# Optimization experiments

Hardware: AMD Instinct MI355X
Metric: run time of the kernel (lower is better)

## Reference

```python
import jax, jax.numpy as jnp
from jax import lax
import numpy as np

B, IMG_H, IMG_W = 8, 256, 512
NUM_CLASSES, P = 20, 32
SCALE, TOPK, IOU_THR = 32.0, 100, 0.5


def conv2d(x, w, b, stride=1, pad=1):
    y = lax.conv_general_dilated(x, w, (stride, stride), [(pad, pad), (pad, pad)],
                                 dimension_numbers=('NCHW', 'OIHW', 'NCHW'))
    return y + b[None, :, None, None]


def bilinear_resize(img, out_h, out_w):
    # img: [..., H, W]; torch F.interpolate(mode='bilinear', align_corners=False)
    H, W = img.shape[-2], img.shape[-1]
    def idx_w(n_in, n_out):
        src = (jnp.arange(n_out, dtype=jnp.float32) + 0.5) * (n_in / n_out) - 0.5
        src = jnp.clip(src, 0.0, n_in - 1)
        i0 = jnp.floor(src).astype(jnp.int32)
        i1 = jnp.minimum(i0 + 1, n_in - 1)
        return i0, i1, src - i0.astype(jnp.float32)
    y0, y1, wy = idx_w(H, out_h)
    x0, x1, wx = idx_w(W, out_w)
    top = img[..., y0, :] * (1.0 - wy)[:, None] + img[..., y1, :] * wy[:, None]
    return top[..., x0] * (1.0 - wx) + top[..., x1] * wx


def generate_anchors(fh, fw):
    ys = (jnp.arange(fh, dtype=jnp.float32) + 0.5) * (IMG_H / fh)
    xs = (jnp.arange(fw, dtype=jnp.float32) + 0.5) * (IMG_W / fw)
    cy, cx = jnp.meshgrid(ys, xs, indexing='ij')
    h = SCALE / 2
    return jnp.stack([cx - h, cy - h, cx + h, cy + h], -1).reshape(-1, 4)


def delta_to_boxes(anchors, deltas):
    a_c = (anchors[:, :2] + anchors[:, 2:]) / 2
    a_wh = anchors[:, 2:] - anchors[:, :2]
    pc = a_c + deltas[..., :2] * a_wh
    pwh = a_wh * jnp.exp(deltas[..., 2:])
    return jnp.concatenate([pc - pwh / 2, pc + pwh / 2], -1)


def nms_single(boxes, scores, labels):
    # torchvision batched_nms: offset boxes per label, greedy NMS, return kept idxs
    N = boxes.shape[0]
    off = labels.astype(boxes.dtype) * (jnp.max(boxes) + 1.0)
    b = boxes + off[:, None]
    order = jnp.argsort(-scores)
    bs = b[order]
    area = (bs[:, 2] - bs[:, 0]) * (bs[:, 3] - bs[:, 1])
    lt = jnp.maximum(bs[:, None, :2], bs[None, :, :2])
    rb = jnp.minimum(bs[:, None, 2:], bs[None, :, 2:])
    wh = jnp.clip(rb - lt, 0.0)
    inter = wh[..., 0] * wh[..., 1]
    iou = inter / (area[:, None] + area[None, :] - inter + 1e-9)
    idxs = jnp.arange(N)
    def body(i, suppressed):
        keep_i = jnp.logical_not(suppressed[i])
        row = (iou[i] > IOU_THR) & (idxs > i)
        return jnp.where(keep_i, suppressed | row, suppressed)
    suppressed = lax.fori_loop(0, N, body, jnp.zeros(N, bool))
    keep_mask = ~suppressed
    rank = jnp.cumsum(keep_mask) - 1
    slots = jnp.where(keep_mask & (rank < TOPK), rank, TOPK)
    out = jnp.full(TOPK + 1, -1, jnp.int32).at[slots].set(order.astype(jnp.int32))
    return out[:TOPK]


def setup_inputs():
    key = jax.random.key(0)
    ks = jax.random.split(key, 17)
    def cw(k, o, i, kh, kw_):
        return jax.random.normal(k, (o, i, kh, kw_), jnp.float32) / np.sqrt(i * kh * kw_)
    return {
        'images': jax.random.normal(ks[0], (B, 3, IMG_H, IMG_W), jnp.float32),
        'w1': cw(ks[1], 64, 3, 3, 3),   'b1': jnp.zeros(64, jnp.float32),
        'w2': cw(ks[2], 128, 64, 3, 3), 'b2': jnp.zeros(128, jnp.float32),
        'w3': cw(ks[3], 256, 128, 3, 3),'b3': jnp.zeros(256, jnp.float32),
        'pw1': cw(ks[4], 256, 256, 3, 3), 'pb1': jnp.zeros(256, jnp.float32),
        'pw2': cw(ks[5], P, 256, 1, 1),   'pb2': jnp.zeros(P, jnp.float32),
        'cw_': cw(ks[6], NUM_CLASSES + 1, 256, 3, 3), 'cb': jnp.zeros(NUM_CLASSES + 1, jnp.float32),
        'bw': cw(ks[7], 4, 256, 3, 3),  'bb': jnp.zeros(4, jnp.float32),
        'kw': cw(ks[8], P, 256, 3, 3),  'kb': jnp.zeros(P, jnp.float32),
    }


def reference(images, w1, b1, w2, b2, w3, b3, pw1, pb1, pw2, pb2, cw_, cb, bw, bb, kw, kb):
    x = jax.nn.relu(conv2d(images, w1, b1, stride=2))
    x = jax.nn.relu(conv2d(x, w2, b2, stride=2))
    feat = jax.nn.relu(conv2d(x, w3, b3, stride=2))          # [B,256,32,64]
    proto = conv2d(jax.nn.relu(conv2d(feat, pw1, pb1)), pw2, pb2, pad=0)  # [B,P,32,64]
    fh, fw = feat.shape[2], feat.shape[3]
    def head(w, b, c):
        return conv2d(feat, w, b).transpose(0, 2, 3, 1).reshape(B, -1, c)
    cls = head(cw_, cb, NUM_CLASSES + 1)     # [B,N,C+1]
    box = head(bw, bb, 4)                    # [B,N,4]
    coef = head(kw, kb, P)                   # [B,N,P]
    anchors = generate_anchors(fh, fw)       # [N,4]
    probs = jax.nn.softmax(cls, -1)[..., :-1]
    scores = probs.max(-1)
    labels = probs.argmax(-1).astype(jnp.int32)
    boxes = delta_to_boxes(anchors, box)     # [B,N,4]
    keep = jax.vmap(nms_single)(boxes, scores, labels)   # [B,100], -1 pad
    valid = keep >= 0
    ki = jnp.clip(keep, 0)
    take = lambda a: jnp.take_along_axis(a, ki[..., None] if a.ndim == 3 else ki, axis=1)
    boxes_k = take(boxes) * valid[..., None]
    scores_k = take(scores) * valid
    labels_k = jnp.where(valid, take(labels), 0)
    coef_k = jnp.take_along_axis(coef, ki[..., None], axis=1)   # [B,100,P]
    m = jax.nn.sigmoid(jnp.einsum('bkp,bphw->bkhw', coef_k, proto))
    masks = bilinear_resize(m, IMG_H, IMG_W) > 0.5
    masks = masks & valid[..., None, None]
    return boxes_k, scores_k, labels_k, masks, valid
```

## Files before the change

### kernel.cpp

```cpp
#include <hip/hip_runtime.h>
#include <hip/hip_bf16.h>
#include <math.h>

#define BB 8
#define NCLS 21
#define NANCH 2048
#define TOPK_N 100

static const size_t OFF_X1HI = 0;
static const size_t OFF_X1LO = 34344960;
static const size_t OFF_X2HI = 68689920;
static const size_t OFF_X2LO = 86261760;
static const size_t OFF_FTHI = 103833600;
static const size_t OFF_FTLO = 113025024;
static const size_t ZERO_BYTES = 122216448;
static const size_t OFF_WT1  = 122216448;
static const size_t OFF_A2H  = 122223616;
static const size_t OFF_A2L  = 122371072;
static const size_t OFF_A3H  = 122518528;
static const size_t OFF_A3L  = 123108352;
static const size_t OFF_AHH  = 123698176;
static const size_t OFF_AHL  = 123993088;
static const size_t OFF_AP1H = 124288000;
static const size_t OFF_AP1L = 125467648;
static const size_t OFF_WTP2 = 126647296;
static const size_t OFF_BH   = 126680064;
static const size_t OFF_HOUT = 126680576;
static const size_t OFF_P1   = 130874880;
static const size_t OFF_PROTO= 147652096;
static const size_t OFF_BOXES= 149749248;
static const size_t OFF_SCORES=150011392;
static const size_t OFF_LABELS=150076928;
static const size_t OFF_ORDER= 150142464;
static const size_t OFF_SB   = 150208000;
static const size_t OFF_IOU  = 150470144;
static const size_t OFF_KEEP = 154664448;
static const size_t OFF_MAXB = 154668032;
static const size_t OFF_M    = 154668544;

static const size_t OUT_BOXES  = 0;
static const size_t OUT_SCORES = 3200;
static const size_t OUT_LABELS = 4000;
static const size_t OUT_MASKS  = 4800;
static const size_t OUT_VALID  = 104862400;

typedef __attribute__((ext_vector_type(8))) short bf16x8;
typedef __attribute__((ext_vector_type(4))) float f32x4;

__device__ __forceinline__ unsigned encf(float f){
  unsigned u = __float_as_uint(f);
  return (u & 0x80000000u) ? ~u : (u | 0x80000000u);
}
__device__ __forceinline__ float decf(unsigned u){
  unsigned b = (u & 0x80000000u) ? (u & 0x7fffffffu) : ~u;
  return __uint_as_float(b);
}
__device__ __forceinline__ short f2bf(float f){
  __hip_bfloat16 h = __float2bfloat16(f);
  return *(short*)&h;
}
__device__ __forceinline__ float bf2f(short h){
  return __uint_as_float(((unsigned)(unsigned short)h) << 16);
}

__global__ void initk(unsigned* maxb){
  if (threadIdx.x < BB) maxb[threadIdx.x] = 0u;
}

__global__ void zerok(float4* __restrict__ p, long n4){
  long i = (long)blockIdx.x*256 + threadIdx.x;
  if (i < n4) p[i] = make_float4(0.f,0.f,0.f,0.f);
}

template<int CIN,int COUT,int KK>
__global__ void packw(const float* __restrict__ w, float* __restrict__ wT){
  int i = blockIdx.x*256 + threadIdx.x;
  if (i >= CIN*KK*COUT) return;
  int co = i % COUT; int r = i / COUT;
  int ci = r / KK,  k = r % KK;
  wT[i] = w[(co*CIN + ci)*KK + k];
}

template<int CIN,int COUT>
__global__ void packA(const float* __restrict__ w, short* __restrict__ Ahi,
                      short* __restrict__ Alo){
  constexpr int K = CIN*9;
  constexpr int KS = K/32;
  int i = blockIdx.x*256 + threadIdx.x;
  if (i >= COUT*K) return;
  int sub  = i & 7;
  int lane = (i >> 3) & 63;
  int rest = i >> 9;
  int ks = rest % KS;
  int mt = rest / KS;
  int m = mt*16 + (lane & 15);
  int k = ks*32 + (lane >> 4)*8 + sub;
  int tap = k / CIN, ci = k - tap*CIN;
  float v = w[(m*CIN + ci)*9 + tap];
  short h = f2bf(v);
  Ahi[i] = h;
  Alo[i] = f2bf(v - bf2f(h));
}

__global__ void packAh(const float* __restrict__ cw, const float* __restrict__ bw,
                       const float* __restrict__ kw, const float* __restrict__ cb,
                       const float* __restrict__ bb, const float* __restrict__ kb,
                       short* __restrict__ Ahi, short* __restrict__ Alo,
                       float* __restrict__ bh){
  int i = blockIdx.x*256 + threadIdx.x;
  if (i < 64){
    float v = 0.f;
    if (i < 21) v = cb[i]; else if (i < 25) v = bb[i-21]; else if (i < 57) v = kb[i-25];
    bh[i] = v;
  }
  if (i >= 64*2304) return;
  constexpr int KS = 72;
  int sub  = i & 7;
  int lane = (i >> 3) & 63;
  int rest = i >> 9;
  int ks = rest % KS;
  int mt = rest / KS;
  int m = mt*16 + (lane & 15);
  int k = ks*32 + (lane >> 4)*8 + sub;
  int tap = k >> 8, ci = k & 255;
  float v = 0.f;
  if (m < 21)      v = cw[(m*256 + ci)*9 + tap];
  else if (m < 25) v = bw[((m-21)*256 + ci)*9 + tap];
  else if (m < 57) v = kw[((m-25)*256 + ci)*9 + tap];
  short h = f2bf(v);
  Ahi[i] = h;
  Alo[i] = f2bf(v - bf2f(h));
}

__global__ __launch_bounds__(256) void conv1k(const float* __restrict__ img,
    const float* __restrict__ wT, const float* __restrict__ bias,
    short* __restrict__ x1hi, short* __restrict__ x1lo){
  const int b   = blockIdx.z;
  const int co0 = blockIdx.y * 16;
  const int g   = blockIdx.x*256 + threadIdx.x;
  const int y  = g >> 7;
  const int x0 = (g & 127) << 1;

  float acc[16][2];
#pragma unroll
  for (int c=0;c<16;c++){
    float bv = bias[co0+c];
    acc[c][0] = bv; acc[c][1] = bv;
  }
  int   off[3][5];
  float msk[3][5];
#pragma unroll
  for (int kh=0;kh<3;kh++){
    int iy = y*2 - 1 + kh;
    bool okr = (iy >= 0) && (iy < 256);
    int ro = okr ? iy*512 : 0;
#pragma unroll
    for (int t=0;t<5;t++){
      int col = x0*2 - 1 + t;
      bool ok = okr && (col >= 0) && (col < 512);
      off[kh][t] = ok ? (ro + col) : 0;
      msk[kh][t] = ok ? 1.f : 0.f;
    }
  }
  const float* inb = img + (size_t)b*3*256*512;
  for (int ci=0; ci<3; ci++){
    const float* inc = inb + (size_t)ci*256*512;
    float v[3][5];
#pragma unroll
    for (int kh=0;kh<3;kh++)
#pragma unroll
      for (int t=0;t<5;t++)
        v[kh][t] = inc[off[kh][t]] * msk[kh][t];
    const float* wp = wT + ci*9*64 + co0;
#pragma unroll
    for (int kh=0;kh<3;kh++)
#pragma unroll
    for (int kw=0;kw<3;kw++){
      const float* wq = wp + (kh*3+kw)*64;
#pragma unroll
      for (int c=0;c<16;c++){
        float wv = wq[c];
        acc[c][0] = fmaf(wv, v[kh][2*0+kw], acc[c][0]);
        acc[c][1] = fmaf(wv, v[kh][2*1+kw], acc[c][1]);
      }
    }
  }
#pragma unroll
  for (int s=0;s<2;s++){
    short hv[16] __attribute__((aligned(16)));
    short lv[16] __attribute__((aligned(16)));
#pragma unroll
    for (int c=0;c<16;c++){
      float r = fmaxf(acc[c][s], 0.f);
      short h = f2bf(r);
      hv[c] = h;
      lv[c] = f2bf(r - bf2f(h));
    }
#pragma unroll
    for (int g2=0; g2<2; g2++){
      size_t ad = (((size_t)(b*8 + (co0>>3) + g2)*130 + (y+1))*258 + (x0+s+1))*8;
      *(bf16x8*)(x1hi + ad) = *(bf16x8*)(hv + g2*8);
      *(bf16x8*)(x1lo + ad) = *(bf16x8*)(lv + g2*8);
    }
  }
}

template<int CIN,int K,int M,int MW,int NW,int OW,int OHh,int S,int IPH,int IPW,
         bool SPLIT,int EMODE,int OPH,int OPW>
__global__ __launch_bounds__(NW*64) void cgemm(
    const short* __restrict__ Ahi, const short* __restrict__ Alo,
    const short* __restrict__ Bhi, const short* __restrict__ Blo,
    const float* __restrict__ bias, float* __restrict__ outf,
    short* __restrict__ outhi, short* __restrict__ outlo){
  static_assert(CIN % 32 == 0, "CIN must be multiple of 32");
  constexpr int NT = OW*OHh;
  constexpr int KS = K/32;
  constexpr int CG = CIN/8;
  const int b    = blockIdx.z;
  const int wave = threadIdx.x >> 6;
  const int lane = threadIdx.x & 63;
  const int lm = lane & 15, lq = lane >> 4;
  const int m0 = (blockIdx.y * NW + wave) * (MW*16);
  const int n0 = blockIdx.x * 64;

  int oy[4], ox[4];
#pragma unroll
  for (int j=0;j<4;j++){
    int n = n0 + j*16 + lm;
    oy[j] = n / OW; ox[j] = n % OW;
  }

  f32x4 acc[MW][4];
#pragma unroll
  for (int i=0;i<MW;i++)
#pragma unroll
    for (int j=0;j<4;j++) acc[i][j] = (f32x4){0.f,0.f,0.f,0.f};

  const short* Ah_l = Ahi + (size_t)lane*8;
  const short* Al_l = Alo + (size_t)lane*8;
  const int mt0 = m0 >> 4;

  const size_t plane = (size_t)IPH*IPW;
  const short* Bh0 = Bhi + ((size_t)b*CG + lq)*plane*8;
  const short* Bl0 = Blo + ((size_t)b*CG + lq)*plane*8;

#pragma unroll 3
  for (int tap=0; tap<9; tap++){
    const int dy = tap/3, dx = tap%3;
    size_t pix[4];
#pragma unroll
    for (int j=0;j<4;j++)
      pix[j] = (size_t)(oy[j]*S + dy)*IPW + (size_t)(ox[j]*S + dx);
    const int ksb = tap*(CIN/32);
#pragma unroll
    for (int kc=0; kc<CIN; kc+=32){
      const int ks = ksb + (kc>>5);
      const size_t koff = (size_t)(kc>>3)*plane;
      bf16x8 ah[MW], bh_[4];
#pragma unroll
      for (int i=0;i<MW;i++)
        ah[i] = *(const bf16x8*)(Ah_l + ((size_t)(mt0+i)*KS + ks)*512);
#pragma unroll
      for (int j=0;j<4;j++) bh_[j] = *(const bf16x8*)(Bh0 + (koff + pix[j])*8);
      if constexpr (SPLIT){
        bf16x8 al[MW], bl_[4];
#pragma unroll
        for (int i=0;i<MW;i++)
          al[i] = *(const bf16x8*)(Al_l + ((size_t)(mt0+i)*KS + ks)*512);
#pragma unroll
        for (int j=0;j<4;j++) bl_[j] = *(const bf16x8*)(Bl0 + (koff + pix[j])*8);
#pragma unroll
        for (int j=0;j<4;j++)
#pragma unroll
          for (int i=0;i<MW;i++)
            acc[i][j] = __builtin_amdgcn_mfma_f32_16x16x32_bf16(ah[i], bh_[j], acc[i][j], 0,0,0);
#pragma unroll
        for (int j=0;j<4;j++)
#pragma unroll
          for (int i=0;i<MW;i++)
            acc[i][j] = __builtin_amdgcn_mfma_f32_16x16x32_bf16(ah[i], bl_[j], acc[i][j], 0,0,0);
#pragma unroll
        for (int j=0;j<4;j++)
#pragma unroll
          for (int i=0;i<MW;i++)
            acc[i][j] = __builtin_amdgcn_mfma_f32_16x16x32_bf16(al[i], bh_[j], acc[i][j], 0,0,0);
      } else {
#pragma unroll
        for (int j=0;j<4;j++)
#pragma unroll
          for (int i=0;i<MW;i++)
            acc[i][j] = __builtin_amdgcn_mfma_f32_16x16x32_bf16(ah[i], bh_[j], acc[i][j], 0,0,0);
      }
    }
  }

#pragma unroll
  for (int i=0;i<MW;i++){
#pragma unroll
    for (int r=0;r<4;r++){
      const int m = m0 + i*16 + lq*4 + r;
      const float bv = bias[m];
      if constexpr (EMODE == 0){
#pragma unroll
        for (int j=0;j<4;j++){
          float v = fmaxf(acc[i][j][r] + bv, 0.f);
          short h = f2bf(v);
          short l = f2bf(v - bf2f(h));
          size_t ad = ((((size_t)(b*(M/8) + (m>>3))*OPH + (oy[j]+1))*OPW + (ox[j]+1)))*8 + (m&7);
          outhi[ad] = h;
          outlo[ad] = l;
        }
      } else {
        float* cp = outf + ((size_t)b*M + m)*NT + n0 + lm;
#pragma unroll
        for (int j=0;j<4;j++){
          float v = acc[i][j][r] + bv;
          if constexpr (EMODE == 2) v = fmaxf(v, 0.f);
          cp[j*16] = v;
        }
      }
    }
  }
}

__global__ __launch_bounds__(256) void pw2k2(const float* __restrict__ p1,
    const float* __restrict__ wT, const float* __restrict__ bias,
    float* __restrict__ proto){
  const int b  = blockIdx.y;
  const int sp = blockIdx.x*256 + threadIdx.x;
  float acc[32];
#pragma unroll
  for (int c=0;c<32;c++) acc[c] = bias[c];
  const float* pb = p1 + (size_t)b*256*NANCH + sp;
  for (int ci=0;ci<256;ci++){
    float v = pb[(size_t)ci*NANCH];
    const float* wq = wT + ci*32;
#pragma unroll
    for (int c=0;c<32;c++) acc[c] = fmaf(v, wq[c], acc[c]);
  }
#pragma unroll
  for (int c=0;c<32;c++)
    proto[((size_t)b*32 + c)*NANCH + sp] = acc[c];
}

__global__ void decodek(const float* __restrict__ hout,
                        float* __restrict__ boxes, float* __restrict__ scores,
                        int* __restrict__ labels, unsigned* __restrict__ maxb){
  const int b = blockIdx.y;
  const int n = blockIdx.x*blockDim.x + threadIdx.x;
  const float* cp = hout + (size_t)b*64*NANCH + n;
  float l[NCLS];
  float M = -1e30f;
#pragma unroll
  for (int c=0;c<NCLS;c++){ l[c] = cp[(size_t)c*NANCH]; M = fmaxf(M, l[c]); }
  float denom = 0.f;
#pragma unroll
  for (int c=0;c<NCLS;c++) denom += expf(l[c]-M);
  float best = -1.f; int bi = 0;
#pragma unroll
  for (int c=0;c<NCLS-1;c++){
    float e = expf(l[c]-M);
    if (e > best){ best = e; bi = c; }
  }
  scores[(size_t)b*NANCH + n] = best/denom;
  labels[(size_t)b*NANCH + n] = bi;

  float dx = cp[21*(size_t)NANCH], dy = cp[22*(size_t)NANCH];
  float dw = cp[23*(size_t)NANCH], dh = cp[24*(size_t)NANCH];
  const int yy = n >> 6, xx = n & 63;
  float cx = (xx+0.5f)*8.f, cy = (yy+0.5f)*8.f;
  float px = cx + dx*32.f, py = cy + dy*32.f;
  float pw = 32.f*expf(dw), ph = 32.f*expf(dh);
  float x1 = px - 0.5f*pw, y1 = py - 0.5f*ph;
  float x2 = px + 0.5f*pw, y2 = py + 0.5f*ph;
  float* bo = boxes + ((size_t)b*NANCH + n)*4;
  bo[0]=x1; bo[1]=y1; bo[2]=x2; bo[3]=y2;
  float mx = fmaxf(fmaxf(x1,y1), fmaxf(x2,y2));
#pragma unroll
  for (int off=32; off>0; off>>=1) mx = fmaxf(mx, __shfl_down(mx, off));
  if ((threadIdx.x & 63) == 0) atomicMax(maxb + b, encf(mx));
}

__global__ void __launch_bounds__(1024) sortk(const float* __restrict__ scores,
                     const float* __restrict__ boxes, const int* __restrict__ labels,
                     const unsigned* __restrict__ maxb,
                     int* __restrict__ order, float* __restrict__ sb){
  __shared__ float sc[NANCH];
  __shared__ int   id[NANCH];
  const int b = blockIdx.x, t = threadIdx.x;
  for (int i=t;i<NANCH;i+=1024){ sc[i]=scores[(size_t)b*NANCH+i]; id[i]=i; }
  __syncthreads();
  for (int k=2;k<=NANCH;k<<=1){
    for (int j=k>>1;j>0;j>>=1){
      for (int i=t;i<NANCH;i+=1024){
        int ixj = i ^ j;
        if (ixj > i){
          float sa=sc[i], sb_=sc[ixj]; int ia=id[i], ib=id[ixj];
          bool dir = ((i & k) == 0);
          bool before_ba = (sb_ > sa) || (sb_ == sa && ib < ia);
          if (before_ba == dir){ sc[i]=sb_; sc[ixj]=sa; id[i]=ib; id[ixj]=ia; }
        }
      }
      __syncthreads();
    }
  }
  float mboff = decf(maxb[b]) + 1.0f;
  for (int r=t;r<NANCH;r+=1024){
    int o = id[r];
    order[(size_t)b*NANCH + r] = o;
    float off = (float)labels[(size_t)b*NANCH + o] * mboff;
    const float* bo = boxes + ((size_t)b*NANCH + o)*4;
    float* sp = sb + ((size_t)b*NANCH + r)*4;
    sp[0]=bo[0]+off; sp[1]=bo[1]+off; sp[2]=bo[2]+off; sp[3]=bo[3]+off;
  }
}

__global__ void ioumask(const float* __restrict__ sb, unsigned long long* __restrict__ iou){
  const int b = blockIdx.y;
  const int gid = blockIdx.x*blockDim.x + threadIdx.x;
  const int i = gid >> 5, w = gid & 31;
  const float* base = sb + (size_t)b*NANCH*4;
  unsigned long long bits = 0ull;
  const int j0 = w << 6;
  if (j0 + 63 > i){
    float x1=base[i*4], y1=base[i*4+1], x2=base[i*4+2], y2=base[i*4+3];
    float ai = (x2-x1)*(y2-y1);
    for (int jj=0;jj<64;jj++){
      int j = j0 + jj;
      if (j > i){
        float bx1=base[j*4], by1=base[j*4+1], bx2=base[j*4+2], by2=base[j*4+3];
        float lx=fmaxf(x1,bx1), ly=fmaxf(y1,by1);
        float rx=fminf(x2,bx2), ry=fminf(y2,by2);
        float ww=fmaxf(rx-lx,0.f), hh=fmaxf(ry-ly,0.f);
        float inter = ww*hh;
        float aj = (bx2-bx1)*(by2-by1);
        float v = inter/(ai + aj - inter + 1e-9f);
        if (v > 0.5f) bits |= (1ull << jj);
      }
    }
  }
  iou[((size_t)b*NANCH + i)*32 + w] = bits;
}

__global__ void nmsscan(const unsigned long long* __restrict__ iou,
                        const int* __restrict__ order, int* __restrict__ keep){
  const int b = blockIdx.x, lane = threadIdx.x;
  unsigned long long sup = 0ull;
  int k = 0;
  for (int i=0; i<NANCH && k<TOPK_N; i++){
    int wi = i >> 6, bi = i & 63;
    unsigned long long wv = __shfl(sup, wi);
    if (!((wv >> bi) & 1ull)){
      if (lane == 0) keep[b*TOPK_N + k] = order[(size_t)b*NANCH + i];
      k++;
      unsigned long long row = (lane < 32) ? iou[((size_t)b*NANCH + i)*32 + lane] : 0ull;
      sup |= row;
    }
  }
  for (int r = lane; r < TOPK_N; r += 64)
    if (r >= k) keep[b*TOPK_N + r] = -1;
}

__global__ void gatherk(const int* __restrict__ keep, const float* __restrict__ boxes,
                        const float* __restrict__ scores, const int* __restrict__ labels,
                        float* __restrict__ out){
  const int b = blockIdx.x, r = threadIdx.x;
  if (r >= TOPK_N) return;
  int ki = keep[b*TOPK_N + r];
  float valid = (ki >= 0) ? 1.f : 0.f;
  int kc = (ki < 0) ? 0 : ki;
  const float* bo = boxes + ((size_t)b*NANCH + kc)*4;
#pragma unroll
  for (int c=0;c<4;c++) out[OUT_BOXES + ((size_t)b*TOPK_N + r)*4 + c] = bo[c]*valid;
  out[OUT_SCORES + b*TOPK_N + r] = scores[(size_t)b*NANCH + kc]*valid;
  out[OUT_LABELS + b*TOPK_N + r] = (ki >= 0) ? (float)labels[(size_t)b*NANCH + kc] : 0.f;
  out[OUT_VALID  + b*TOPK_N + r] = valid;
}

__global__ void maskm(const int* __restrict__ keep, const float* __restrict__ hout,
                      const float* __restrict__ proto, float* __restrict__ m){
  const int b = blockIdx.z, r = blockIdx.y;
  const int s = blockIdx.x*blockDim.x + threadIdx.x;
  __shared__ float cf[32];
  int ki = keep[b*TOPK_N + r];
  int kc = (ki < 0) ? 0 : ki;
  if (threadIdx.x < 32)
    cf[threadIdx.x] = hout[((size_t)b*64 + 25 + threadIdx.x)*NANCH + kc];
  __syncthreads();
  float acc = 0.f;
#pragma unroll
  for (int p=0;p<32;p++) acc = fmaf(cf[p], proto[((size_t)b*32 + p)*NANCH + s], acc);
  m[((size_t)b*TOPK_N + r)*NANCH + s] = 1.f/(1.f + expf(-acc));
}

__global__ void resizek(const float* __restrict__ m, const int* __restrict__ keep,
                        float* __restrict__ out){
  const int b = blockIdx.z, r = blockIdx.y;
  const int pid = blockIdx.x*blockDim.x + threadIdx.x;
  const int y  = pid >> 7;
  const int x4 = (pid & 127) << 2;
  bool valid = keep[b*TOPK_N + r] >= 0;
  const float* mb = m + ((size_t)b*TOPK_N + r)*NANCH;
  float sy = (y + 0.5f)*0.125f - 0.5f;
  sy = fminf(fmaxf(sy, 0.f), 31.f);
  int y0 = (int)floorf(sy);
  int y1 = min(y0+1, 31);
  float wy = sy - (float)y0;
  const float* r0 = mb + y0*64;
  const float* r1 = mb + y1*64;
  float res[4];
#pragma unroll
  for (int k=0;k<4;k++){
    int x = x4 + k;
    float sx = (x + 0.5f)*0.125f - 0.5f;
    sx = fminf(fmaxf(sx, 0.f), 63.f);
    int x0 = (int)floorf(sx);
    int x1 = min(x0+1, 63);
    float wx = sx - (float)x0;
    float t0 = r0[x0]*(1.f-wy) + r1[x0]*wy;
    float t1 = r0[x1]*(1.f-wy) + r1[x1]*wy;
    float v  = t0*(1.f-wx) + t1*wx;
    res[k] = (v > 0.5f && valid) ? 1.f : 0.f;
  }
  float4 v4 = make_float4(res[0], res[1], res[2], res[3]);
  *(float4*)(out + OUT_MASKS + (((size_t)b*TOPK_N + r)*256 + y)*512 + x4) = v4;
}

extern "C" void kernel_launch(void* const* d_in, const int* in_sizes, int n_in,
                              void* d_out, int out_size, void* d_ws, size_t ws_size,
                              hipStream_t stream) {
  const float* images=(const float*)d_in[0];
  const float* w1=(const float*)d_in[1];  const float* b1=(const float*)d_in[2];
  const float* w2=(const float*)d_in[3];  const float* b2=(const float*)d_in[4];
  const float* w3=(const float*)d_in[5];  const float* b3=(const float*)d_in[6];
  const float* pw1=(const float*)d_in[7]; const float* pb1=(const float*)d_in[8];
  const float* pw2=(const float*)d_in[9]; const float* pb2=(const float*)d_in[10];
  const float* cw=(const float*)d_in[11]; const float* cb=(const float*)d_in[12];
  const float* bw=(const float*)d_in[13]; const float* bb=(const float*)d_in[14];
  const float* kw=(const float*)d_in[15]; const float* kb=(const float*)d_in[16];
  float* out = (float*)d_out;
  char* ws = (char*)d_ws;

  short* x1hi = (short*)(ws + OFF_X1HI);
  short* x1lo = (short*)(ws + OFF_X1LO);
  short* x2hi = (short*)(ws + OFF_X2HI);
  short* x2lo = (short*)(ws + OFF_X2LO);
  short* fthi = (short*)(ws + OFF_FTHI);
  short* ftlo = (short*)(ws + OFF_FTLO);
  float* wT1  = (float*)(ws + OFF_WT1);
  short* a2h  = (short*)(ws + OFF_A2H);
  short* a2l  = (short*)(ws + OFF_A2L);
  short* a3h  = (short*)(ws + OFF_A3H);
  short* a3l  = (short*)(ws + OFF_A3L);
  short* ahh  = (short*)(ws + OFF_AHH);
  short* ahl  = (short*)(ws + OFF_AHL);
  short* ap1h = (short*)(ws + OFF_AP1H);
  short* ap1l = (short*)(ws + OFF_AP1L);
  float* wTp2 = (float*)(ws + OFF_WTP2);
  float* bh   = (float*)(ws + OFF_BH);
  float* hout = (float*)(ws + OFF_HOUT);
  float* p1   = (float*)(ws + OFF_P1);
  float* proto= (float*)(ws + OFF_PROTO);
  float* boxes= (float*)(ws + OFF_BOXES);
  float* scores=(float*)(ws + OFF_SCORES);
  int*   labels=(int*)  (ws + OFF_LABELS);
  int*   order =(int*)  (ws + OFF_ORDER);
  float* sb   = (float*)(ws + OFF_SB);
  unsigned long long* iou = (unsigned long long*)(ws + OFF_IOU);
  int*   keep = (int*)  (ws + OFF_KEEP);
  unsigned* maxb = (unsigned*)(ws + OFF_MAXB);
  float* m    = (float*)(ws + OFF_M);

  initk<<<dim3(1), dim3(64), 0, stream>>>(maxb);

  zerok<<<dim3((unsigned)(ZERO_BYTES/16/256)), 256, 0, stream>>>((float4*)ws, (long)(ZERO_BYTES/16));

  packw<3,64,9>  <<<dim3(7),    256, 0, stream>>>(w1, wT1);
  packA<64,128>  <<<dim3(288),  256, 0, stream>>>(w2, a2h, a2l);
  packA<128,256> <<<dim3(1152), 256, 0, stream>>>(w3, a3h, a3l);
  packA<256,256> <<<dim3(2304), 256, 0, stream>>>(pw1, ap1h, ap1l);
  packAh<<<dim3(576), 256, 0, stream>>>(cw, bw, kw, cb, bb, kb, ahh, ahl, bh);
  packw<256,32,1><<<dim3(32),   256, 0, stream>>>(pw2, wTp2);

  conv1k<<<dim3(64,4,BB), 256, 0, stream>>>(images, wT1, b1, x1hi, x1lo);

  cgemm<64,576,128,4,2,128,64,2,130,258,true,0,66,130>
      <<<dim3(128,1,BB), 128, 0, stream>>>(a2h, a2l, x1hi, x1lo, b2, nullptr, x2hi, x2lo);

  cgemm<128,1152,256,4,4,64,32,2,66,130,true,0,34,66>
      <<<dim3(32,1,BB), 256, 0, stream>>>(a3h, a3l, x2hi, x2lo, b3, nullptr, fthi, ftlo);

  cgemm<256,2304,64,2,2,64,32,1,34,66,true,1,1,1>
      <<<dim3(32,1,BB), 128, 0, stream>>>(ahh, ahl, fthi, ftlo, bh, hout, nullptr, nullptr);

  cgemm<256,2304,256,4,4,64,32,1,34,66,false,2,1,1>
      <<<dim3(32,1,BB), 256, 0, stream>>>(ap1h, ap1l, fthi, fthi, pb1, p1, nullptr, nullptr);

  pw2k2<<<dim3(8,BB), 256, 0, stream>>>(p1, wTp2, pb2, proto);

  decodek<<<dim3(8,BB), 256, 0, stream>>>(hout, boxes, scores, labels, maxb);
  sortk<<<dim3(BB), 1024, 0, stream>>>(scores, boxes, labels, maxb, order, sb);
  ioumask<<<dim3(256,BB), 256, 0, stream>>>(sb, iou);
  nmsscan<<<dim3(BB), 64, 0, stream>>>(iou, order, keep);
  gatherk<<<dim3(BB), 128, 0, stream>>>(keep, boxes, scores, labels, out);

  maskm<<<dim3(8,TOPK_N,BB), 256, 0, stream>>>(keep, hout, proto, m);
  resizek<<<dim3(128,TOPK_N,BB), 256, 0, stream>>>(m, keep, out);
}
```

Before: 1.017 ms.

## Add row-tiled conv GEMM staging input rows in LDS and retile layers

Adds a cgemm_row kernel in which each block handles one output row. For each dy it stages the hi part of the three input rows into shared memory, then reads the B fragments from LDS instead of global memory. Layers 3, the heads and proto1 now use this kernel with M split across more blocks, and layer 2 changes its MW/NW tiling. The separate initk launch is also folded into zerok. The row kernel adds __syncthreads barriers and more LDS use, and the lo part of the input is still read from global memory.

```diff
diff --git a/kernel.cpp b/kernel.cpp
--- a/kernel.cpp
+++ b/kernel.cpp
@@ -63,12 +63,9 @@
   return __uint_as_float(((unsigned)(unsigned short)h) << 16);
 }
 
-__global__ void initk(unsigned* maxb){
-  if (threadIdx.x < BB) maxb[threadIdx.x] = 0u;
-}
-
-__global__ void zerok(float4* __restrict__ p, long n4){
+__global__ void zerok(float4* __restrict__ p, long n4, unsigned* __restrict__ maxb){
   long i = (long)blockIdx.x*256 + threadIdx.x;
+  if (i < BB) maxb[i] = 0u;
   if (i < n4) p[i] = make_float4(0.f,0.f,0.f,0.f);
 }
 
@@ -312,6 +309,138 @@
         }
       } else {
         float* cp = outf + ((size_t)b*M + m)*NT + n0 + lm;
+#pragma unroll
+        for (int j=0;j<4;j++){
+          float v = acc[i][j][r] + bv;
+          if constexpr (EMODE == 2) v = fmaxf(v, 0.f);
+          cp[j*16] = v;
+        }
+      }
+    }
+  }
+}
+
+template<int CIN,int K,int M,int MW,int NW,int S,int IPH,int IPW,
+         bool SPLIT,int EMODE,int OPH,int OPW>
+__global__ __launch_bounds__(NW*64) void cgemm_row(
+    const short* __restrict__ Ahi, const short* __restrict__ Alo,
+    const short* __restrict__ Bhi, const short* __restrict__ Blo,
+    const float* __restrict__ bias, float* __restrict__ outf,
+    short* __restrict__ outhi, short* __restrict__ outlo){
+  static_assert(CIN % 32 == 0, "CIN must be multiple of 32");
+  constexpr int NT = 64*32;
+  constexpr int KS = K/32;
+  constexpr int CG = CIN/8;
+  __shared__ short sB[CG*IPW*8];
+
+  const int b    = blockIdx.z;
+  const int oy   = blockIdx.x;
+  const int wave = threadIdx.x >> 6;
+  const int lane = threadIdx.x & 63;
+  const int lm = lane & 15, lq = lane >> 4;
+  const int m0 = (blockIdx.y * NW + wave) * (MW*16);
+  const int tid = threadIdx.x;
+
+  int ox[4];
+#pragma unroll
+  for (int j=0;j<4;j++) ox[j] = j*16 + lm;
+
+  f32x4 acc[MW][4];
+#pragma unroll
+  for (int i=0;i<MW;i++)
+#pragma unroll
+    for (int j=0;j<4;j++) acc[i][j] = (f32x4){0.f,0.f,0.f,0.f};
+
+  const short* Ah_l = Ahi + (size_t)lane*8;
+  const short* Al_l = Alo + (size_t)lane*8;
+  const int mt0 = m0 >> 4;
+  const size_t plane = (size_t)IPH*IPW;
+  const short* Bl0 = Blo + ((size_t)b*CG + lq)*plane*8;
+
+#pragma unroll 1
+  for (int dy=0; dy<3; dy++){
+    const int iy = oy*S + dy;
+    __syncthreads();
+    {
+      const short* srch = Bhi + ((size_t)b*CG*IPH + iy)*IPW*8;
+      for (int c = tid; c < CG*IPW; c += NW*64){
+        int g = c / IPW, p = c - g*IPW;
+        *(bf16x8*)(&sB[(g*IPW + p)*8]) =
+          *(const bf16x8*)(srch + ((size_t)g*plane + p)*8);
+      }
+    }
+    __syncthreads();
+#pragma unroll
+    for (int dx=0; dx<3; dx++){
+      const int tap = dy*3 + dx;
+      const int ksb = tap*(CIN/32);
+#pragma unroll
+      for (int kc=0; kc<CIN; kc+=32){
+        const int ks = ksb + (kc>>5);
+        bf16x8 ah[MW], bh_[4];
+#pragma unroll
+        for (int i=0;i<MW;i++)
+          ah[i] = *(const bf16x8*)(Ah_l + ((size_t)(mt0+i)*KS + ks)*512);
+#pragma unroll
+        for (int j=0;j<4;j++){
+          int p = ox[j]*S + dx;
+          bh_[j] = *(const bf16x8*)(&sB[(((kc>>3) + lq)*IPW + p)*8]);
+        }
+        if constexpr (SPLIT){
+          const size_t koff = (size_t)(kc>>3)*plane;
+          bf16x8 al[MW], bl_[4];
+#pragma unroll
+          for (int i=0;i<MW;i++)
+            al[i] = *(const bf16x8*)(Al_l + ((size_t)(mt0+i)*KS + ks)*512);
+#pragma unroll
+          for (int j=0;j<4;j++){
+            size_t pix = (size_t)iy*IPW + (size_t)(ox[j]*S + dx);
+            bl_[j] = *(const bf16x8*)(Bl0 + (koff + pix)*8);
+          }
+#pragma unroll
+          for (int j=0;j<4;j++)
+#pragma unroll
+            for (int i=0;i<MW;i++)
+              acc[i][j] = __builtin_amdgcn_mfma_f32_16x16x32_bf16(ah[i], bh_[j], acc[i][j], 0,0,0);
+#pragma unroll
+          for (int j=0;j<4;j++)
+#pragma unroll
+            for (int i=0;i<MW;i++)
+              acc[i][j] = __builtin_amdgcn_mfma_f32_16x16x32_bf16(ah[i], bl_[j], acc[i][j], 0,0,0);
+#pragma unroll
+          for (int j=0;j<4;j++)
+#pragma unroll
+            for (int i=0;i<MW;i++)
+              acc[i][j] = __builtin_amdgcn_mfma_f32_16x16x32_bf16(al[i], bh_[j], acc[i][j], 0,0,0);
+        } else {
+#pragma unroll
+          for (int j=0;j<4;j++)
+#pragma unroll
+            for (int i=0;i<MW;i++)
+              acc[i][j] = __builtin_amdgcn_mfma_f32_16x16x32_bf16(ah[i], bh_[j], acc[i][j], 0,0,0);
+        }
+      }
+    }
+  }
+
+#pragma unroll
+  for (int i=0;i<MW;i++){
+#pragma unroll
+    for (int r=0;r<4;r++){
+      const int m = m0 + i*16 + lq*4 + r;
+      const float bv = bias[m];
+      if constexpr (EMODE == 0){
+#pragma unroll
+        for (int j=0;j<4;j++){
+          float v = fmaxf(acc[i][j][r] + bv, 0.f);
+          short h = f2bf(v);
+          short l = f2bf(v - bf2f(h));
+          size_t ad = ((((size_t)(b*(M/8) + (m>>3))*OPH + (oy+1))*OPW + (ox[j]+1)))*8 + (m&7);
+          outhi[ad] = h;
+          outlo[ad] = l;
+        }
+      } else {
+        float* cp = outf + ((size_t)b*M + m)*NT + oy*64 + lm;
 #pragma unroll
         for (int j=0;j<4;j++){
           float v = acc[i][j][r] + bv;
@@ -571,9 +700,7 @@
   unsigned* maxb = (unsigned*)(ws + OFF_MAXB);
   float* m    = (float*)(ws + OFF_M);
 
-  initk<<<dim3(1), dim3(64), 0, stream>>>(maxb);
-
-  zerok<<<dim3((unsigned)(ZERO_BYTES/16/256)), 256, 0, stream>>>((float4*)ws, (long)(ZERO_BYTES/16));
+  zerok<<<dim3((unsigned)(ZERO_BYTES/16/256)), 256, 0, stream>>>((float4*)ws, (long)(ZERO_BYTES/16), maxb);
 
   packw<3,64,9>  <<<dim3(7),    256, 0, stream>>>(w1, wT1);
   packA<64,128>  <<<dim3(288),  256, 0, stream>>>(w2, a2h, a2l);
@@ -584,17 +711,17 @@
 
   conv1k<<<dim3(64,4,BB), 256, 0, stream>>>(images, wT1, b1, x1hi, x1lo);
 
-  cgemm<64,576,128,4,2,128,64,2,130,258,true,0,66,130>
-      <<<dim3(128,1,BB), 128, 0, stream>>>(a2h, a2l, x1hi, x1lo, b2, nullptr, x2hi, x2lo);
-
-  cgemm<128,1152,256,4,4,64,32,2,66,130,true,0,34,66>
-      <<<dim3(32,1,BB), 256, 0, stream>>>(a3h, a3l, x2hi, x2lo, b3, nullptr, fthi, ftlo);
-
-  cgemm<256,2304,64,2,2,64,32,1,34,66,true,1,1,1>
+  cgemm<64,576,128,2,4,128,64,2,130,258,true,0,66,130>
+      <<<dim3(128,1,BB), 256, 0, stream>>>(a2h, a2l, x1hi, x1lo, b2, nullptr, x2hi, x2lo);
+
+  cgemm_row<128,1152,256,2,4,2,66,130,true,0,34,66>
+      <<<dim3(32,2,BB), 256, 0, stream>>>(a3h, a3l, x2hi, x2lo, b3, nullptr, fthi, ftlo);
+
+  cgemm_row<256,2304,64,2,2,1,34,66,true,1,1,1>
       <<<dim3(32,1,BB), 128, 0, stream>>>(ahh, ahl, fthi, ftlo, bh, hout, nullptr, nullptr);
 
-  cgemm<256,2304,256,4,4,64,32,1,34,66,false,2,1,1>
-      <<<dim3(32,1,BB), 256, 0, stream>>>(ap1h, ap1l, fthi, fthi, pb1, p1, nullptr, nullptr);
+  cgemm_row<256,2304,256,2,4,1,34,66,false,2,1,1>
+      <<<dim3(32,2,BB), 256, 0, stream>>>(ap1h, ap1l, fthi, fthi, pb1, p1, nullptr, nullptr);
 
   pw2k2<<<dim3(8,BB), 256, 0, stream>>>(p1, wTp2, pb2, proto);
 
```

Result: no change. 1.006 ms (-1.1%).
